# Optimization experiments

Measured on AMD Instinct MI355X. Metric: run time of the kernel, lower is better.

Reference implementation:

```python
import jax, jax.numpy as jnp
import numpy as np

DIM = 384
HEADS = 8
RATES = (0.5, 0.75)  # sparse_rates
EPS = 1e-12  # torch F.normalize default eps


def _dwconv3x3(x, w):
    # depthwise 3x3, padding=1; w: [3*dim, 1, 3, 3]
    return jax.lax.conv_general_dilated(
        x, w, window_strides=(1, 1), padding=((1, 1), (1, 1)),
        feature_group_count=w.shape[0],
        dimension_numbers=('NCHW', 'OIHW', 'NCHW'))


def setup_inputs() -> dict:
    key = jax.random.key(0)
    ks = jax.random.split(key, 5)
    dim = DIM
    x = jax.random.normal(ks[0], (4, dim, 128, 128), jnp.float32)
    qkv_w = jax.random.normal(ks[1], (3 * dim, dim), jnp.float32) * 0.05   # 1x1 conv
    dw_w = jax.random.normal(ks[2], (3 * dim, 1, 3, 3), jnp.float32) * 0.1  # depthwise 3x3
    proj_w = jax.random.normal(ks[3], (dim, dim), jnp.float32) * 0.05       # 1x1 conv
    temperature = jnp.ones((HEADS, 1, 1), jnp.float32)
    attns = jnp.full((len(RATES),), 0.2, jnp.float32)
    return {"x": x, "qkv_w": qkv_w, "dw_w": dw_w, "proj_w": proj_w,
            "temperature": temperature, "attns": attns}


def reference(x, qkv_w, dw_w, proj_w, temperature, attns) -> jnp.ndarray:
    b, c, h, w = x.shape
    qkv = jnp.einsum('bchw,oc->bohw', x, qkv_w)  # 1x1 conv, no bias
    qkv = _dwconv3x3(qkv, dw_w)
    q, k, v = jnp.split(qkv, 3, axis=1)

    def heads(t):  # b (head c) h w -> b head c (h w)
        return t.reshape(b, HEADS, c // HEADS, h * w)

    q, k, v = heads(q), heads(k), heads(v)
    q = q / jnp.maximum(jnp.linalg.norm(q, axis=-1, keepdims=True), EPS)
    k = k / jnp.maximum(jnp.linalg.norm(k, axis=-1, keepdims=True), EPS)
    C = q.shape[2]
    attn = jnp.einsum('bhcn,bhdn->bhcd', q, k) * temperature  # [b, head, C, C]

    out = jnp.zeros_like(v)  # [b, head, C, HW]
    for i, rate in enumerate(RATES):
        kk = int(C * rate)
        _, idx = jax.lax.top_k(attn, kk)                      # [b, head, C, kk]
        mask = jax.nn.one_hot(idx, C, dtype=attn.dtype).sum(-2) > 0  # scatter 1s
        attn = jnp.where(mask, attn, -jnp.inf)
        attn = jax.nn.softmax(attn, axis=-1)  # NOTE: original reuses softmaxed attn next iter
        out = out + jnp.einsum('bhcd,bhdn->bhcn', attn, v) * attns[i]

    out = out.reshape(b, c, h, w)  # b head c (hw) -> b (head c) h w
    return jnp.einsum('bchw,oc->bohw', out, proj_w)
```

## Files before the change

### kernel.cpp

```cpp
#include <hip/hip_runtime.h>
#include <math.h>

#define HW     16384
#define WIDTH  128
#define CDIM   384
#define QKVC   1152
#define HEADS  8
#define CH     48
#define NSPLIT 32
#define GK     384

typedef unsigned short u16;
typedef short bf16x8 __attribute__((ext_vector_type(8)));
typedef u16 u16x8 __attribute__((ext_vector_type(8)));
typedef float f32x4 __attribute__((ext_vector_type(4)));

__device__ __forceinline__ void split2(float x, u16& h, u16& l) {
    union { float f; unsigned u; } a, b, c;
    a.f = x;
    unsigned hu = (a.u + 0x7fffu + ((a.u >> 16) & 1u)) & 0xffff0000u;
    b.u = hu;
    h = (u16)(hu >> 16);
    c.f = x - b.f;
    l = (u16)((c.u + 0x7fffu + ((c.u >> 16) & 1u)) >> 16);
}

__device__ __forceinline__ void gload16(const void* g, void* l) {
    __builtin_amdgcn_global_load_lds((const __attribute__((address_space(1))) unsigned int*)g,
                                     (__attribute__((address_space(3))) unsigned int*)l, 16, 0, 0);
}

__global__ __launch_bounds__(256)
void mfma_gemm(const u16* __restrict__ Ah, const u16* __restrict__ Al,
               const u16* __restrict__ Bh, const u16* __restrict__ Bl,
               float* __restrict__ C, int nmb,
               long abs_, long bbs, long cbs)
{
    extern __shared__ char smem[];
    const int tot = gridDim.x * gridDim.y;
    const int per = tot >> 3;
    const int fl  = blockIdx.x + gridDim.x * blockIdx.y;
    const int f2  = (fl & 7) * per + (fl >> 3);
    const int nblk = f2 / nmb, mblk = f2 % nmb;
    const int b = blockIdx.z;
    Ah += (long)b * abs_; Al += (long)b * abs_;
    Bh += (long)b * bbs;  Bl += (long)b * bbs;
    C  += (long)b * cbs;
    const int m0 = mblk * 128, n0 = nblk * 128;

    const int tid  = threadIdx.x;
    const int wave = tid >> 6, lane = tid & 63;
    const int lr = lane & 15, lg = lane >> 4;
    const int wm = wave >> 1, wn = wave & 1;

    const int srow = tid >> 2;
    const int kc   = tid & 3;
    const int sw   = kc ^ ((srow >> 1) & 3);

    f32x4 acc[4][4];
#pragma unroll
    for (int i = 0; i < 4; ++i)
#pragma unroll
        for (int j = 0; j < 4; ++j) acc[i][j] = (f32x4){0.f, 0.f, 0.f, 0.f};

#define STAGE(bs, kt) do { char* LL = smem + (bs) * 32768;                          \
        const long ko = (long)(kt) * 32 + sw * 8;                                   \
        gload16(Ah + (long)(m0 + srow) * GK      + ko, LL + tid * 16);              \
        gload16(Ah + (long)(m0 + 64 + srow) * GK + ko, LL + 4096  + tid * 16);      \
        gload16(Al + (long)(m0 + srow) * GK      + ko, LL + 8192  + tid * 16);      \
        gload16(Al + (long)(m0 + 64 + srow) * GK + ko, LL + 12288 + tid * 16);      \
        gload16(Bh + (long)(n0 + srow) * GK      + ko, LL + 16384 + tid * 16);      \
        gload16(Bh + (long)(n0 + 64 + srow) * GK + ko, LL + 20480 + tid * 16);      \
        gload16(Bl + (long)(n0 + srow) * GK      + ko, LL + 24576 + tid * 16);      \
        gload16(Bl + (long)(n0 + 64 + srow) * GK + ko, LL + 28672 + tid * 16);      \
    } while (0)

    STAGE(0, 0);
    STAGE(1, 1);
#pragma unroll
    for (int kt = 0; kt < 12; ++kt) {
        if (kt < 11) asm volatile("s_waitcnt vmcnt(8)" ::: "memory");
        else         asm volatile("s_waitcnt vmcnt(0)" ::: "memory");
        __builtin_amdgcn_s_barrier();

        const char* L = smem + (kt & 1) * 32768;
        bf16x8 af[4][2], bf[4][2];
#pragma unroll
        for (int mi = 0; mi < 4; ++mi) {
            int r = wm * 64 + mi * 16 + lr;
            int off = r * 64 + (((lg ^ (r >> 1)) & 3) << 4);
            af[mi][0] = *(const bf16x8*)(L + off);
            af[mi][1] = *(const bf16x8*)(L + 8192 + off);
        }
#pragma unroll
        for (int ni = 0; ni < 4; ++ni) {
            int r = wn * 64 + ni * 16 + lr;
            int off = r * 64 + (((lg ^ (r >> 1)) & 3) << 4);
            bf[ni][0] = *(const bf16x8*)(L + 16384 + off);
            bf[ni][1] = *(const bf16x8*)(L + 24576 + off);
        }
        asm volatile("s_waitcnt lgkmcnt(0)" ::: "memory");
        __builtin_amdgcn_sched_barrier(0);
        __builtin_amdgcn_s_barrier();
        if (kt + 2 < 12) STAGE(kt & 1, kt + 2);

        __builtin_amdgcn_s_setprio(1);
#pragma unroll
        for (int mi = 0; mi < 4; ++mi)
#pragma unroll
            for (int ni = 0; ni < 4; ++ni) {
                acc[mi][ni] = __builtin_amdgcn_mfma_f32_16x16x32_bf16(af[mi][0], bf[ni][0], acc[mi][ni], 0, 0, 0);
                acc[mi][ni] = __builtin_amdgcn_mfma_f32_16x16x32_bf16(af[mi][0], bf[ni][1], acc[mi][ni], 0, 0, 0);
                acc[mi][ni] = __builtin_amdgcn_mfma_f32_16x16x32_bf16(af[mi][1], bf[ni][0], acc[mi][ni], 0, 0, 0);
            }
        __builtin_amdgcn_s_setprio(0);
    }
#undef STAGE

#pragma unroll
    for (int mi = 0; mi < 4; ++mi)
#pragma unroll
        for (int ni = 0; ni < 4; ++ni) {
            int row = m0 + wm * 64 + mi * 16 + lg * 4;
            int col = n0 + wn * 64 + ni * 16 + lr;
            float* cp = C + (long)row * HW + col;
            cp[0]          = acc[mi][ni][0];
            cp[(long)HW]   = acc[mi][ni][1];
            cp[2L * HW]    = acc[mi][ni][2];
            cp[3L * HW]    = acc[mi][ni][3];
        }
}

__global__ __launch_bounds__(256)
void convT_kernel(const float* __restrict__ in, u16* __restrict__ oh, u16* __restrict__ ol,
                  long ibs, long obs)
{
    const int b = blockIdx.z;
    in += (long)b * ibs; oh += (long)b * obs; ol += (long)b * obs;
    __shared__ float t[32][33];
    const int p0 = blockIdx.x * 32, c0 = blockIdx.y * 32;
    const int ty = threadIdx.x >> 5, tx = threadIdx.x & 31;
#pragma unroll
    for (int it = 0; it < 4; ++it) {
        int c = ty + it * 8;
        t[c][tx] = in[(long)(c0 + c) * HW + p0 + tx];
    }
    __syncthreads();
    const int cp = threadIdx.x & 15;
    const int py = threadIdx.x >> 4;
#pragma unroll
    for (int half = 0; half < 2; ++half) {
        int p = py + half * 16;
        u16 h0, l0, h1, l1;
        split2(t[2 * cp][p], h0, l0);
        split2(t[2 * cp + 1][p], h1, l1);
        long o = (long)(p0 + p) * CDIM + c0 + 2 * cp;
        *(ushort2*)&oh[o] = (ushort2){h0, h1};
        *(ushort2*)&ol[o] = (ushort2){l0, l1};
    }
}

__global__ __launch_bounds__(256)
void convA_kernel(const float* __restrict__ in, u16* __restrict__ oh, u16* __restrict__ ol, int n)
{
    int i = blockIdx.x * 256 + threadIdx.x;
    if (i < n) split2(in[i], oh[i], ol[i]);
}

__global__ __launch_bounds__(256)
void dwconv_kernel(const float* __restrict__ in, const float* __restrict__ w,
                   float* __restrict__ out)
{
    const long base = (long)blockIdx.y * QKVC * HW;
    const int idx = blockIdx.x * 256 + threadIdx.x;
    const int ch = idx >> 11;
    const int wi = idx & 2047;
    const int y = wi >> 4, x0 = (wi & 15) * 8;
    const float* wp = w + ch * 9;
    const float* ip = in + base + (long)ch * HW;
    float o[8] = {0.f, 0.f, 0.f, 0.f, 0.f, 0.f, 0.f, 0.f};
#pragma unroll
    for (int dy = -1; dy <= 1; ++dy) {
        int yy = y + dy;
        if ((unsigned)yy >= 128u) continue;
        const float* rp = ip + yy * WIDTH + x0;
        float4 a  = *(const float4*)rp;
        float4 bq = *(const float4*)(rp + 4);
        float v[10] = { (x0 > 0) ? rp[-1] : 0.f,
                        a.x, a.y, a.z, a.w, bq.x, bq.y, bq.z, bq.w,
                        (x0 < 120) ? rp[8] : 0.f };
        float w0 = wp[(dy + 1) * 3], w1 = wp[(dy + 1) * 3 + 1], w2 = wp[(dy + 1) * 3 + 2];
#pragma unroll
        for (int j = 0; j < 8; ++j)
            o[j] = fmaf(w0, v[j], fmaf(w1, v[j + 1], fmaf(w2, v[j + 2], o[j])));
    }
    float* op = out + base + (long)ch * HW + y * WIDTH + x0;
    *(float4*)op       = (float4){o[0], o[1], o[2], o[3]};
    *(float4*)(op + 4) = (float4){o[4], o[5], o[6], o[7]};
}

__global__ __launch_bounds__(256)
void dwconv_vT_kernel(const float* __restrict__ in, const float* __restrict__ w,
                      u16* __restrict__ oh, u16* __restrict__ ol, long ibs, long obs)
{
    const int b  = blockIdx.z;
    const int cg = blockIdx.y;
    const int p0 = blockIdx.x * 64;
    const int y  = p0 >> 7, xh = p0 & 127;
    __shared__ unsigned pk[64][97];

    const int tid = threadIdx.x;
    const int seg = tid & 7;
    const int chl = tid >> 3;
    const int x0  = xh + seg * 8;
#pragma unroll
    for (int cp = 0; cp < 3; ++cp) {
        const int cl = cp * 32 + chl;
        const int c  = cg * 96 + cl;
        const float* ip = in + (long)b * ibs + (long)(768 + c) * HW;
        const float* wp = w + (768 + c) * 9;
        float o[8] = {0.f, 0.f, 0.f, 0.f, 0.f, 0.f, 0.f, 0.f};
#pragma unroll
        for (int dy = -1; dy <= 1; ++dy) {
            int yy = y + dy;
            if ((unsigned)yy >= 128u) continue;
            const float* rp = ip + yy * WIDTH + x0;
            float4 a  = *(const float4*)rp;
            float4 bq = *(const float4*)(rp + 4);
            float v[10] = { (x0 > 0) ? rp[-1] : 0.f,
                            a.x, a.y, a.z, a.w, bq.x, bq.y, bq.z, bq.w,
                            (x0 < 120) ? rp[8] : 0.f };
            float w0 = wp[(dy + 1) * 3], w1 = wp[(dy + 1) * 3 + 1], w2 = wp[(dy + 1) * 3 + 2];
#pragma unroll
            for (int j = 0; j < 8; ++j)
                o[j] = fmaf(w0, v[j], fmaf(w1, v[j + 1], fmaf(w2, v[j + 2], o[j])));
        }
#pragma unroll
        for (int j = 0; j < 8; ++j) {
            u16 hh, ll;
            split2(o[j], hh, ll);
            pk[seg * 8 + j][cl] = ((unsigned)hh << 16) | ll;
        }
    }
    __syncthreads();
    const int px = tid >> 2, qt = tid & 3;
    u16 hs[24], ls[24];
#pragma unroll
    for (int j = 0; j < 24; ++j) {
        unsigned v = pk[px][qt * 24 + j];
        hs[j] = (u16)(v >> 16);
        ls[j] = (u16)(v & 0xffffu);
    }
    u16* ph = oh + (long)b * obs + (long)(p0 + px) * CDIM + cg * 96 + qt * 24;
    u16* pl = ol + (long)b * obs + (long)(p0 + px) * CDIM + cg * 96 + qt * 24;
#pragma unroll
    for (int j = 0; j < 3; ++j) {
        *(u16x8*)(ph + j * 8) = *(const u16x8*)&hs[j * 8];
        *(u16x8*)(pl + j * 8) = *(const u16x8*)&ls[j * 8];
    }
}

__global__ __launch_bounds__(256)
void attn_partial_kernel(const float* __restrict__ dw, float* __restrict__ part,
                         float* __restrict__ part2, long ps, long p2s)
{
    const int split = blockIdx.x, h = blockIdx.y, b = blockIdx.z;
    const int n0 = split * (HW / NSPLIT);
    const float* qbase = dw + ((long)b * QKVC + h * CH) * HW;
    const float* kbase = dw + ((long)b * QKVC + CDIM + h * CH) * HW;
    __shared__ float qs[64][CH];
    __shared__ float ks[64][CH];
    const int tid = threadIdx.x;
    const int tr = tid >> 4, tc = tid & 15;
    const int c0 = tr * 3, d0 = tc * 3;
    float acc[3][3] = {{0.f}};
    float qss[3] = {0.f, 0.f, 0.f}, kss[3] = {0.f, 0.f, 0.f};
    const int cA = tid >> 4;
    const int nq = (tid & 15) * 4;
    for (int ns = 0; ns < HW / NSPLIT; ns += 64) {
        __syncthreads();
#pragma unroll
        for (int t = 0; t < 3; ++t) {
            int c = cA + t * 16;
            float4 qv = *(const float4*)(qbase + (long)c * HW + n0 + ns + nq);
            float4 kv = *(const float4*)(kbase + (long)c * HW + n0 + ns + nq);
            qs[nq + 0][c] = qv.x; qs[nq + 1][c] = qv.y;
            qs[nq + 2][c] = qv.z; qs[nq + 3][c] = qv.w;
            ks[nq + 0][c] = kv.x; ks[nq + 1][c] = kv.y;
            ks[nq + 2][c] = kv.z; ks[nq + 3][c] = kv.w;
            qss[t] += qv.x * qv.x + qv.y * qv.y + qv.z * qv.z + qv.w * qv.w;
            kss[t] += kv.x * kv.x + kv.y * kv.y + kv.z * kv.z + kv.w * kv.w;
        }
        __syncthreads();
#pragma unroll 8
        for (int n = 0; n < 64; ++n) {
            float q0 = qs[n][c0], q1 = qs[n][c0 + 1], q2 = qs[n][c0 + 2];
            float k0 = ks[n][d0], k1 = ks[n][d0 + 1], k2 = ks[n][d0 + 2];
            acc[0][0] = fmaf(q0, k0, acc[0][0]); acc[0][1] = fmaf(q0, k1, acc[0][1]); acc[0][2] = fmaf(q0, k2, acc[0][2]);
            acc[1][0] = fmaf(q1, k0, acc[1][0]); acc[1][1] = fmaf(q1, k1, acc[1][1]); acc[1][2] = fmaf(q1, k2, acc[1][2]);
            acc[2][0] = fmaf(q2, k0, acc[2][0]); acc[2][1] = fmaf(q2, k1, acc[2][1]); acc[2][2] = fmaf(q2, k2, acc[2][2]);
        }
    }
#pragma unroll
    for (int m = 1; m < 16; m <<= 1) {
#pragma unroll
        for (int t = 0; t < 3; ++t) {
            qss[t] += __shfl_xor(qss[t], m);
            kss[t] += __shfl_xor(kss[t], m);
        }
    }
    if ((tid & 15) == 0) {
        float* p2 = part2 + (long)b * p2s + ((long)h * NSPLIT + split) * 96;
#pragma unroll
        for (int t = 0; t < 3; ++t) {
            p2[cA + t * 16]      = qss[t];
            p2[48 + cA + t * 16] = kss[t];
        }
    }
    float* po = part + (long)b * ps + ((long)h * NSPLIT + split) * (CH * CH);
#pragma unroll
    for (int i = 0; i < 3; ++i)
#pragma unroll
        for (int j = 0; j < 3; ++j)
            po[(c0 + i) * CH + d0 + j] = acc[i][j];
}

__global__ __launch_bounds__(256)
void attn_reduce_kernel(const float* __restrict__ part, const float* __restrict__ part2,
                        const float* __restrict__ temp, float* __restrict__ attn,
                        long ps, long p2s, long as_)
{
    const int seg = blockIdx.x, h = blockIdx.y, b = blockIdx.z;
    const float* pp = part + (long)b * ps + (long)h * NSPLIT * (CH * CH);
    const float* p2 = part2 + (long)b * p2s + (long)h * NSPLIT * 96;
    __shared__ float sinv[96];
    if (threadIdx.x < 96) {
        float s = 0.f;
        for (int sp = 0; sp < NSPLIT; ++sp) s += p2[sp * 96 + threadIdx.x];
        sinv[threadIdx.x] = 1.f / fmaxf(sqrtf(s), 1e-12f);
    }
    __syncthreads();
    const float t = temp[h];
    const int idx = seg * 256 + threadIdx.x;
    const int c = idx / CH, d = idx % CH;
    float s = 0.f;
    for (int sp = 0; sp < NSPLIT; ++sp) s += pp[sp * (CH * CH) + idx];
    attn[(long)b * as_ + (long)h * (CH * CH) + idx] = s * sinv[c] * sinv[48 + d] * t;
}

__global__ __launch_bounds__(256)
void maskw_kernel(const float* __restrict__ attn, const float* __restrict__ attns,
                  float* __restrict__ W, long as_, long ws_)
{
    const int h = blockIdx.y, b = blockIdx.z;
    const int wave = threadIdx.x >> 6, lane = threadIdx.x & 63;
    const int r = blockIdx.x * 4 + wave;
    const float* ap = attn + (long)b * as_ + (long)h * (CH * CH) + (long)r * CH;
    float a = (lane < CH) ? ap[lane] : -3.4e38f;

    int rank = 0;
#pragma unroll
    for (int j = 0; j < CH; ++j) {
        float aj = __shfl(a, j);
        rank += (aj > a) || (aj == a && j < lane);
    }
    const bool keep = (lane < CH) && (rank < 24);
    float m = keep ? a : -3.4e38f;
#pragma unroll
    for (int o = 32; o > 0; o >>= 1) m = fmaxf(m, __shfl_xor(m, o));
    float e = keep ? expf(a - m) : 0.f;
    float s = e;
#pragma unroll
    for (int o = 32; o > 0; o >>= 1) s += __shfl_xor(s, o);
    const float A1 = e / s;

    int rank2 = 0;
#pragma unroll
    for (int j = 0; j < CH; ++j) {
        float aj = __shfl(A1, j);
        rank2 += (aj > A1) || (aj == A1 && j < lane);
    }
    const bool keep2 = (lane < CH) && (rank2 < 36);
    float m2 = keep2 ? A1 : -3.4e38f;
#pragma unroll
    for (int o = 32; o > 0; o >>= 1) m2 = fmaxf(m2, __shfl_xor(m2, o));
    float e2 = keep2 ? expf(A1 - m2) : 0.f;
    float s2 = e2;
#pragma unroll
    for (int o = 32; o > 0; o >>= 1) s2 += __shfl_xor(s2, o);

    if (lane < CH)
        W[(long)b * ws_ + (long)h * (CH * CH) + (long)r * CH + lane] =
            attns[0] * A1 + attns[1] * (e2 / s2);
}

__global__ __launch_bounds__(256)
void mbuild_kernel(const float* __restrict__ P, const float* __restrict__ W,
                   u16* __restrict__ Mh, u16* __restrict__ Ml, long ws_, long ms)
{
    const int b = blockIdx.y;
    const int idx = blockIdx.x * 256 + threadIdx.x;
    const int o = idx / CDIM, col = idx % CDIM;
    const int h = col / CH, d = col % CH;
    const float* wp = W + (long)b * ws_ + (long)h * (CH * CH) + d;
    const float* pp = P + (long)o * CDIM + h * CH;
    float s = 0.f;
#pragma unroll
    for (int c = 0; c < CH; ++c) s = fmaf(pp[c], wp[c * CH], s);
    u16 hh, ll;
    split2(s, hh, ll);
    Mh[(long)b * ms + idx] = hh;
    Ml[(long)b * ms + idx] = ll;
}

extern "C" void kernel_launch(void* const* d_in, const int* in_sizes, int n_in,
                              void* d_out, int out_size, void* d_ws, size_t ws_size,
                              hipStream_t stream)
{
    const float* x      = (const float*)d_in[0];
    const float* qkv_w  = (const float*)d_in[1];
    const float* dw_w   = (const float*)d_in[2];
    const float* proj_w = (const float*)d_in[3];
    const float* temp   = (const float*)d_in[4];
    const float* attns  = (const float*)d_in[5];
    float* out = (float*)d_out;

    const size_t perbB = (size_t)QKVC * HW * 4;
    auto need = [&](int nb) -> size_t {
        return (size_t)nb * 2 * perbB + 4u * QKVC * CDIM + 4096;
    };
    int NB = 4;
    while (NB > 1 && need(NB) > ws_size) NB >>= 1;

    const long fstride = (long)(perbB / 4);
    const long ustride = (long)(perbB / 2);

    const size_t PART_B  = 27u << 20;
    const size_t PART2_B = (29u << 20) + (512u << 10);
    const size_t ATT_B   = 30u << 20;
    const size_t WM_B    = 31u << 20;
    const size_t MH_B    = 32u << 20;
    const size_t ML_B    = 33u << 20;

    char* buf1 = (char*)d_ws;
    char* buf2 = buf1 + (size_t)NB * perbB;
    u16* Ah = (u16*)(buf2 + (size_t)NB * perbB);
    u16* Al = Ah + (size_t)QKVC * CDIM;

    convA_kernel<<<dim3((QKVC * CDIM + 255) / 256), 256, 0, stream>>>(qkv_w, Ah, Al, QKVC * CDIM);

    for (int b0 = 0; b0 < 4; b0 += NB) {
        const int nb = NB;
        float* pre = (float*)buf1;
        float* dwb = (float*)buf2;
        u16* xt_h = (u16*)buf2;                u16* xt_l = xt_h + (size_t)HW * CDIM;
        u16* vt_h = (u16*)(dwb + (size_t)768 * HW);
        u16* vt_l = vt_h + (size_t)CDIM * HW;
        float* part  = (float*)(buf1 + PART_B);
        float* part2 = (float*)(buf1 + PART2_B);
        float* attn  = (float*)(buf1 + ATT_B);
        float* Wm    = (float*)(buf1 + WM_B);
        u16* Mh = (u16*)(buf1 + MH_B);
        u16* Ml = (u16*)(buf1 + ML_B);

        convT_kernel<<<dim3(HW / 32, CDIM / 32, nb), 256, 0, stream>>>(
            x + (size_t)b0 * CDIM * HW, xt_h, xt_l, (long)CDIM * HW, ustride);
        mfma_gemm<<<dim3(HW / 128, QKVC / 128, nb), 256, 65536, stream>>>(
            Ah, Al, xt_h, xt_l, pre, QKVC / 128, 0L, ustride, fstride);
        dwconv_kernel<<<dim3(768 * HW / 8 / 256, nb), 256, 0, stream>>>(pre, dw_w, dwb);
        dwconv_vT_kernel<<<dim3(HW / 64, 4, nb), 256, 0, stream>>>(pre, dw_w, vt_h, vt_l,
                                                                   fstride, ustride);
        attn_partial_kernel<<<dim3(NSPLIT, HEADS, nb), 256, 0, stream>>>(dwb, part, part2,
                                                                         fstride, fstride);
        attn_reduce_kernel<<<dim3(9, HEADS, nb), 256, 0, stream>>>(part, part2, temp, attn,
                                                                   fstride, fstride, fstride);
        maskw_kernel<<<dim3(12, HEADS, nb), 256, 0, stream>>>(attn, attns, Wm, fstride, fstride);
        mbuild_kernel<<<dim3(CDIM * CDIM / 256, nb), 256, 0, stream>>>(proj_w, Wm, Mh, Ml,
                                                                       fstride, ustride);
        mfma_gemm<<<dim3(HW / 128, CDIM / 128, nb), 256, 65536, stream>>>(
            Mh, Ml, vt_h, vt_l, out + (size_t)b0 * CDIM * HW, CDIM / 128,
            ustride, ustride, (long)CDIM * HW);
    }
}
```

Measured before the change: 635.1 us.

## Widen GEMM tile to 128x256 and fuse q/k depthwise conv into attention partials

The MFMA GEMM now computes 128x256 output tiles per block, with a larger LDS double buffer and staged LDS-wait/MFMA interleaving. This is meant to improve operand reuse and overlap the next stage's loads with the last MFMA group. Separately, the standalone depthwise conv for q and k is removed, and attn_partial_kernel applies the 3x3 conv on the fly from the pre-conv buffer. That avoids writing and re-reading a large intermediate, at the cost of redundant halo reads. Workspace pointers move to buf2 so they do not alias the pre buffer. The larger tile raises register and LDS use, which may reduce occupancy.

```diff
diff --git a/kernel.cpp b/kernel.cpp
--- a/kernel.cpp
+++ b/kernel.cpp
@@ -46,45 +46,60 @@
     Ah += (long)b * abs_; Al += (long)b * abs_;
     Bh += (long)b * bbs;  Bl += (long)b * bbs;
     C  += (long)b * cbs;
-    const int m0 = mblk * 128, n0 = nblk * 128;
+    const int m0 = mblk * 128, n0 = nblk * 256;
 
     const int tid  = threadIdx.x;
     const int wave = tid >> 6, lane = tid & 63;
     const int lr = lane & 15, lg = lane >> 4;
     const int wm = wave >> 1, wn = wave & 1;
 
-    const int srow = tid >> 2;
-    const int kc   = tid & 3;
-    const int sw   = kc ^ ((srow >> 1) & 3);
-
-    f32x4 acc[4][4];
+    const int s  = tid >> 2;
+    const int sw = (tid & 3) ^ ((tid >> 3) & 3);
+
+    f32x4 acc[4][8];
 #pragma unroll
     for (int i = 0; i < 4; ++i)
 #pragma unroll
-        for (int j = 0; j < 4; ++j) acc[i][j] = (f32x4){0.f, 0.f, 0.f, 0.f};
-
-#define STAGE(bs, kt) do { char* LL = smem + (bs) * 32768;                          \
-        const long ko = (long)(kt) * 32 + sw * 8;                                   \
-        gload16(Ah + (long)(m0 + srow) * GK      + ko, LL + tid * 16);              \
-        gload16(Ah + (long)(m0 + 64 + srow) * GK + ko, LL + 4096  + tid * 16);      \
-        gload16(Al + (long)(m0 + srow) * GK      + ko, LL + 8192  + tid * 16);      \
-        gload16(Al + (long)(m0 + 64 + srow) * GK + ko, LL + 12288 + tid * 16);      \
-        gload16(Bh + (long)(n0 + srow) * GK      + ko, LL + 16384 + tid * 16);      \
-        gload16(Bh + (long)(n0 + 64 + srow) * GK + ko, LL + 20480 + tid * 16);      \
-        gload16(Bl + (long)(n0 + srow) * GK      + ko, LL + 24576 + tid * 16);      \
-        gload16(Bl + (long)(n0 + 64 + srow) * GK + ko, LL + 28672 + tid * 16);      \
+        for (int j = 0; j < 8; ++j) acc[i][j] = (f32x4){0.f, 0.f, 0.f, 0.f};
+
+#define STAGE(bs, kt) do { char* LL = smem + (bs) * 49152;                        \
+        const long ko = (long)(kt) * 32 + sw * 8;                                 \
+        gload16(Ah + (long)(m0 + s) * GK + ko,        LL + 0     + tid * 16);     \
+        gload16(Ah + (long)(m0 + 64 + s) * GK + ko,   LL + 4096  + tid * 16);     \
+        gload16(Al + (long)(m0 + s) * GK + ko,        LL + 8192  + tid * 16);     \
+        gload16(Al + (long)(m0 + 64 + s) * GK + ko,   LL + 12288 + tid * 16);     \
+        gload16(Bh + (long)(n0 + s) * GK + ko,        LL + 16384 + tid * 16);     \
+        gload16(Bh + (long)(n0 + 64 + s) * GK + ko,   LL + 20480 + tid * 16);     \
+        gload16(Bh + (long)(n0 + 128 + s) * GK + ko,  LL + 24576 + tid * 16);     \
+        gload16(Bh + (long)(n0 + 192 + s) * GK + ko,  LL + 28672 + tid * 16);     \
+        gload16(Bl + (long)(n0 + s) * GK + ko,        LL + 32768 + tid * 16);     \
+        gload16(Bl + (long)(n0 + 64 + s) * GK + ko,   LL + 36864 + tid * 16);     \
+        gload16(Bl + (long)(n0 + 128 + s) * GK + ko,  LL + 40960 + tid * 16);     \
+        gload16(Bl + (long)(n0 + 192 + s) * GK + ko,  LL + 45056 + tid * 16);     \
+    } while (0)
+
+#define MFMA2(NI0, NI1) do {                                                                      \
+        _Pragma("unroll")                                                                         \
+        for (int mi = 0; mi < 4; ++mi) {                                                          \
+            acc[mi][NI0] = __builtin_amdgcn_mfma_f32_16x16x32_bf16(af[mi][0], bf[NI0][0], acc[mi][NI0], 0, 0, 0); \
+            acc[mi][NI0] = __builtin_amdgcn_mfma_f32_16x16x32_bf16(af[mi][0], bf[NI0][1], acc[mi][NI0], 0, 0, 0); \
+            acc[mi][NI0] = __builtin_amdgcn_mfma_f32_16x16x32_bf16(af[mi][1], bf[NI0][0], acc[mi][NI0], 0, 0, 0); \
+            acc[mi][NI1] = __builtin_amdgcn_mfma_f32_16x16x32_bf16(af[mi][0], bf[NI1][0], acc[mi][NI1], 0, 0, 0); \
+            acc[mi][NI1] = __builtin_amdgcn_mfma_f32_16x16x32_bf16(af[mi][0], bf[NI1][1], acc[mi][NI1], 0, 0, 0); \
+            acc[mi][NI1] = __builtin_amdgcn_mfma_f32_16x16x32_bf16(af[mi][1], bf[NI1][0], acc[mi][NI1], 0, 0, 0); \
+        }                                                                                         \
     } while (0)
 
     STAGE(0, 0);
     STAGE(1, 1);
 #pragma unroll
     for (int kt = 0; kt < 12; ++kt) {
-        if (kt < 11) asm volatile("s_waitcnt vmcnt(8)" ::: "memory");
+        if (kt < 11) asm volatile("s_waitcnt vmcnt(12)" ::: "memory");
         else         asm volatile("s_waitcnt vmcnt(0)" ::: "memory");
         __builtin_amdgcn_s_barrier();
 
-        const char* L = smem + (kt & 1) * 32768;
-        bf16x8 af[4][2], bf[4][2];
+        const char* L = smem + (kt & 1) * 49152;
+        bf16x8 af[4][2], bf[8][2];
 #pragma unroll
         for (int mi = 0; mi < 4; ++mi) {
             int r = wm * 64 + mi * 16 + lr;
@@ -93,36 +108,48 @@
             af[mi][1] = *(const bf16x8*)(L + 8192 + off);
         }
 #pragma unroll
-        for (int ni = 0; ni < 4; ++ni) {
-            int r = wn * 64 + ni * 16 + lr;
+        for (int ni = 0; ni < 2; ++ni) {
+            int r = wn * 128 + ni * 16 + lr;
             int off = r * 64 + (((lg ^ (r >> 1)) & 3) << 4);
             bf[ni][0] = *(const bf16x8*)(L + 16384 + off);
-            bf[ni][1] = *(const bf16x8*)(L + 24576 + off);
-        }
+            bf[ni][1] = *(const bf16x8*)(L + 32768 + off);
+        }
+        __builtin_amdgcn_sched_barrier(0);
+#pragma unroll
+        for (int ni = 2; ni < 8; ++ni) {
+            int r = wn * 128 + ni * 16 + lr;
+            int off = r * 64 + (((lg ^ (r >> 1)) & 3) << 4);
+            bf[ni][0] = *(const bf16x8*)(L + 16384 + off);
+            bf[ni][1] = *(const bf16x8*)(L + 32768 + off);
+        }
+        __builtin_amdgcn_sched_barrier(0);
+
+        __builtin_amdgcn_s_setprio(1);
+        asm volatile("s_waitcnt lgkmcnt(12)" ::: "memory");
+        __builtin_amdgcn_sched_barrier(0);
+        MFMA2(0, 1);
+        asm volatile("s_waitcnt lgkmcnt(8)" ::: "memory");
+        __builtin_amdgcn_sched_barrier(0);
+        MFMA2(2, 3);
+        asm volatile("s_waitcnt lgkmcnt(4)" ::: "memory");
+        __builtin_amdgcn_sched_barrier(0);
+        MFMA2(4, 5);
         asm volatile("s_waitcnt lgkmcnt(0)" ::: "memory");
         __builtin_amdgcn_sched_barrier(0);
         __builtin_amdgcn_s_barrier();
-        if (kt + 2 < 12) STAGE(kt & 1, kt + 2);
-
-        __builtin_amdgcn_s_setprio(1);
-#pragma unroll
-        for (int mi = 0; mi < 4; ++mi)
-#pragma unroll
-            for (int ni = 0; ni < 4; ++ni) {
-                acc[mi][ni] = __builtin_amdgcn_mfma_f32_16x16x32_bf16(af[mi][0], bf[ni][0], acc[mi][ni], 0, 0, 0);
-                acc[mi][ni] = __builtin_amdgcn_mfma_f32_16x16x32_bf16(af[mi][0], bf[ni][1], acc[mi][ni], 0, 0, 0);
-                acc[mi][ni] = __builtin_amdgcn_mfma_f32_16x16x32_bf16(af[mi][1], bf[ni][0], acc[mi][ni], 0, 0, 0);
-            }
+        if (kt < 10) STAGE(kt & 1, kt + 2);
+        MFMA2(6, 7);
         __builtin_amdgcn_s_setprio(0);
     }
 #undef STAGE
+#undef MFMA2
 
 #pragma unroll
     for (int mi = 0; mi < 4; ++mi)
 #pragma unroll
-        for (int ni = 0; ni < 4; ++ni) {
+        for (int ni = 0; ni < 8; ++ni) {
             int row = m0 + wm * 64 + mi * 16 + lg * 4;
-            int col = n0 + wn * 64 + ni * 16 + lr;
+            int col = n0 + wn * 128 + ni * 16 + lr;
             float* cp = C + (long)row * HW + col;
             cp[0]          = acc[mi][ni][0];
             cp[(long)HW]   = acc[mi][ni][1];
@@ -165,38 +192,6 @@
 {
     int i = blockIdx.x * 256 + threadIdx.x;
     if (i < n) split2(in[i], oh[i], ol[i]);
-}
-
-__global__ __launch_bounds__(256)
-void dwconv_kernel(const float* __restrict__ in, const float* __restrict__ w,
-                   float* __restrict__ out)
-{
-    const long base = (long)blockIdx.y * QKVC * HW;
-    const int idx = blockIdx.x * 256 + threadIdx.x;
-    const int ch = idx >> 11;
-    const int wi = idx & 2047;
-    const int y = wi >> 4, x0 = (wi & 15) * 8;
-    const float* wp = w + ch * 9;
-    const float* ip = in + base + (long)ch * HW;
-    float o[8] = {0.f, 0.f, 0.f, 0.f, 0.f, 0.f, 0.f, 0.f};
-#pragma unroll
-    for (int dy = -1; dy <= 1; ++dy) {
-        int yy = y + dy;
-        if ((unsigned)yy >= 128u) continue;
-        const float* rp = ip + yy * WIDTH + x0;
-        float4 a  = *(const float4*)rp;
-        float4 bq = *(const float4*)(rp + 4);
-        float v[10] = { (x0 > 0) ? rp[-1] : 0.f,
-                        a.x, a.y, a.z, a.w, bq.x, bq.y, bq.z, bq.w,
-                        (x0 < 120) ? rp[8] : 0.f };
-        float w0 = wp[(dy + 1) * 3], w1 = wp[(dy + 1) * 3 + 1], w2 = wp[(dy + 1) * 3 + 2];
-#pragma unroll
-        for (int j = 0; j < 8; ++j)
-            o[j] = fmaf(w0, v[j], fmaf(w1, v[j + 1], fmaf(w2, v[j + 2], o[j])));
-    }
-    float* op = out + base + (long)ch * HW + y * WIDTH + x0;
-    *(float4*)op       = (float4){o[0], o[1], o[2], o[3]};
-    *(float4*)(op + 4) = (float4){o[4], o[5], o[6], o[7]};
 }
 
 __global__ __launch_bounds__(256)
@@ -261,35 +256,70 @@
 }
 
 __global__ __launch_bounds__(256)
-void attn_partial_kernel(const float* __restrict__ dw, float* __restrict__ part,
-                         float* __restrict__ part2, long ps, long p2s)
+void attn_partial_kernel(const float* __restrict__ pre, const float* __restrict__ w,
+                         float* __restrict__ part, float* __restrict__ part2,
+                         long ps, long p2s)
 {
     const int split = blockIdx.x, h = blockIdx.y, b = blockIdx.z;
     const int n0 = split * (HW / NSPLIT);
-    const float* qbase = dw + ((long)b * QKVC + h * CH) * HW;
-    const float* kbase = dw + ((long)b * QKVC + CDIM + h * CH) * HW;
     __shared__ float qs[64][CH];
     __shared__ float ks[64][CH];
     const int tid = threadIdx.x;
     const int tr = tid >> 4, tc = tid & 15;
     const int c0 = tr * 3, d0 = tc * 3;
+    const int cA = tid >> 4;
+    const int nq = (tid & 15) * 4;
+
+    float wq[3][9], wk[3][9];
+#pragma unroll
+    for (int t = 0; t < 3; ++t) {
+        const float* aw = w + ((long)h * CH + cA + t * 16) * 9;
+        const float* bw = w + ((long)CDIM + h * CH + cA + t * 16) * 9;
+#pragma unroll
+        for (int j = 0; j < 9; ++j) { wq[t][j] = aw[j]; wk[t][j] = bw[j]; }
+    }
+
     float acc[3][3] = {{0.f}};
     float qss[3] = {0.f, 0.f, 0.f}, kss[3] = {0.f, 0.f, 0.f};
-    const int cA = tid >> 4;
-    const int nq = (tid & 15) * 4;
+
     for (int ns = 0; ns < HW / NSPLIT; ns += 64) {
+        const int p = n0 + ns;
+        const int y = p >> 7, xh = p & 127;
+        const int x0 = xh + nq;
         __syncthreads();
 #pragma unroll
         for (int t = 0; t < 3; ++t) {
-            int c = cA + t * 16;
-            float4 qv = *(const float4*)(qbase + (long)c * HW + n0 + ns + nq);
-            float4 kv = *(const float4*)(kbase + (long)c * HW + n0 + ns + nq);
-            qs[nq + 0][c] = qv.x; qs[nq + 1][c] = qv.y;
-            qs[nq + 2][c] = qv.z; qs[nq + 3][c] = qv.w;
-            ks[nq + 0][c] = kv.x; ks[nq + 1][c] = kv.y;
-            ks[nq + 2][c] = kv.z; ks[nq + 3][c] = kv.w;
-            qss[t] += qv.x * qv.x + qv.y * qv.y + qv.z * qv.z + qv.w * qv.w;
-            kss[t] += kv.x * kv.x + kv.y * kv.y + kv.z * kv.z + kv.w * kv.w;
+            const int c = cA + t * 16;
+            const float* qp = pre + ((long)b * QKVC + (long)h * CH + c) * HW;
+            const float* kp = qp + (long)CDIM * HW;
+            float oq[4] = {0.f, 0.f, 0.f, 0.f};
+            float ok[4] = {0.f, 0.f, 0.f, 0.f};
+#pragma unroll
+            for (int dy = -1; dy <= 1; ++dy) {
+                int yy = y + dy;
+                if ((unsigned)yy >= 128u) continue;
+                const float* rq = qp + yy * WIDTH + x0;
+                const float* rk = kp + yy * WIDTH + x0;
+                float4 mq = *(const float4*)rq;
+                float4 mk = *(const float4*)rk;
+                float vq[6] = { (x0 > 0) ? rq[-1] : 0.f, mq.x, mq.y, mq.z, mq.w,
+                                (x0 < 124) ? rq[4] : 0.f };
+                float vk[6] = { (x0 > 0) ? rk[-1] : 0.f, mk.x, mk.y, mk.z, mk.w,
+                                (x0 < 124) ? rk[4] : 0.f };
+                float a0 = wq[t][(dy + 1) * 3], a1 = wq[t][(dy + 1) * 3 + 1], a2 = wq[t][(dy + 1) * 3 + 2];
+                float b0 = wk[t][(dy + 1) * 3], b1 = wk[t][(dy + 1) * 3 + 1], b2 = wk[t][(dy + 1) * 3 + 2];
+#pragma unroll
+                for (int j = 0; j < 4; ++j) {
+                    oq[j] = fmaf(a0, vq[j], fmaf(a1, vq[j + 1], fmaf(a2, vq[j + 2], oq[j])));
+                    ok[j] = fmaf(b0, vk[j], fmaf(b1, vk[j + 1], fmaf(b2, vk[j + 2], ok[j])));
+                }
+            }
+            qs[nq + 0][c] = oq[0]; qs[nq + 1][c] = oq[1];
+            qs[nq + 2][c] = oq[2]; qs[nq + 3][c] = oq[3];
+            ks[nq + 0][c] = ok[0]; ks[nq + 1][c] = ok[1];
+            ks[nq + 2][c] = ok[2]; ks[nq + 3][c] = ok[3];
+            qss[t] += oq[0] * oq[0] + oq[1] * oq[1] + oq[2] * oq[2] + oq[3] * oq[3];
+            kss[t] += ok[0] * ok[0] + ok[1] * ok[1] + ok[2] * ok[2] + ok[3] * ok[3];
         }
         __syncthreads();
 #pragma unroll 8
@@ -452,32 +482,30 @@
     for (int b0 = 0; b0 < 4; b0 += NB) {
         const int nb = NB;
         float* pre = (float*)buf1;
-        float* dwb = (float*)buf2;
         u16* xt_h = (u16*)buf2;                u16* xt_l = xt_h + (size_t)HW * CDIM;
-        u16* vt_h = (u16*)(dwb + (size_t)768 * HW);
+        u16* vt_h = (u16*)((float*)buf2 + (size_t)768 * HW);
         u16* vt_l = vt_h + (size_t)CDIM * HW;
-        float* part  = (float*)(buf1 + PART_B);
-        float* part2 = (float*)(buf1 + PART2_B);
-        float* attn  = (float*)(buf1 + ATT_B);
-        float* Wm    = (float*)(buf1 + WM_B);
-        u16* Mh = (u16*)(buf1 + MH_B);
-        u16* Ml = (u16*)(buf1 + ML_B);
+        float* part  = (float*)(buf2 + PART_B);
+        float* part2 = (float*)(buf2 + PART2_B);
+        float* attn  = (float*)(buf2 + ATT_B);
+        float* Wm    = (float*)(buf2 + WM_B);
+        u16* Mh = (u16*)(buf2 + MH_B);
+        u16* Ml = (u16*)(buf2 + ML_B);
 
         convT_kernel<<<dim3(HW / 32, CDIM / 32, nb), 256, 0, stream>>>(
             x + (size_t)b0 * CDIM * HW, xt_h, xt_l, (long)CDIM * HW, ustride);
-        mfma_gemm<<<dim3(HW / 128, QKVC / 128, nb), 256, 65536, stream>>>(
+        mfma_gemm<<<dim3(HW / 256, QKVC / 128, nb), 256, 98304, stream>>>(
             Ah, Al, xt_h, xt_l, pre, QKVC / 128, 0L, ustride, fstride);
-        dwconv_kernel<<<dim3(768 * HW / 8 / 256, nb), 256, 0, stream>>>(pre, dw_w, dwb);
         dwconv_vT_kernel<<<dim3(HW / 64, 4, nb), 256, 0, stream>>>(pre, dw_w, vt_h, vt_l,
                                                                    fstride, ustride);
-        attn_partial_kernel<<<dim3(NSPLIT, HEADS, nb), 256, 0, stream>>>(dwb, part, part2,
+        attn_partial_kernel<<<dim3(NSPLIT, HEADS, nb), 256, 0, stream>>>(pre, dw_w, part, part2,
                                                                          fstride, fstride);
         attn_reduce_kernel<<<dim3(9, HEADS, nb), 256, 0, stream>>>(part, part2, temp, attn,
                                                                    fstride, fstride, fstride);
         maskw_kernel<<<dim3(12, HEADS, nb), 256, 0, stream>>>(attn, attns, Wm, fstride, fstride);
         mbuild_kernel<<<dim3(CDIM * CDIM / 256, nb), 256, 0, stream>>>(proj_w, Wm, Mh, Ml,
                                                                        fstride, ustride);
-        mfma_gemm<<<dim3(HW / 128, CDIM / 128, nb), 256, 65536, stream>>>(
+        mfma_gemm<<<dim3(HW / 256, CDIM / 128, nb), 256, 98304, stream>>>(
             Mh, Ml, vt_h, vt_l, out + (size_t)b0 * CDIM * HW, CDIM / 128,
             ustride, ustride, (long)CDIM * HW);
     }
```

After: 725.9 us. 14.3% more time.
